# Performance work log

Hardware: AMD Instinct MI355X
Metric: run time of the kernel (lower is better)

The kernel has to match this reference:

```python
import jax, jax.numpy as jnp
import numpy as np

# static config (matches init_kwargs)
B, Q, D, H, L, P, V, T = 4, 32, 512, 8, 4, 4, 12000, 16
HD = D // H                      # attn_feat_dim = d_model / n_heads
TS = [2048, 1024, 512, 256]      # temporal_shapes (1-D feature pyramid)
LS = [0, 2048, 3072, 3584]       # level_start_index
S = sum(TS)


def setup_inputs() -> dict:
    key = jax.random.key(0)
    ks = jax.random.split(key, 20)
    f = jnp.float32
    def n(k, shape, s=0.02):
        return jax.random.normal(k, shape, dtype=f) * s
    return dict(
        seq_tokens=jax.random.randint(ks[0], (B * Q, T), 0, V),
        decoder_hidden_states=n(ks[1], (B, Q, D), 1.0),
        reference_points=jax.random.uniform(ks[2], (B, Q, 1), dtype=f),
        enc=n(ks[3], (B, S, D), 1.0),
        valid_ratios=jnp.ones((B, L), dtype=f),
        mask_flatten=jnp.zeros((B, S), dtype=bool),
        temporal_shapes=jnp.array(TS, dtype=jnp.int32),
        level_start_index=jnp.array(LS, dtype=jnp.int32),
        embed_W=jax.random.uniform(ks[4], (V, D), dtype=f, minval=-0.1, maxval=0.1),
        logit_W=jax.random.uniform(ks[5], (V, D), dtype=f, minval=-0.1, maxval=0.1),
        logit_b=jnp.zeros((V,), f),
        Wih=n(ks[6], (4 * D, 3 * D)),   # LSTM weight_ih (no bias), gate order i,f,g,o
        Whh=n(ks[7], (4 * D, D)),       # LSTM weight_hh
        value_W=n(ks[8], (D, D)), value_b=jnp.zeros((D,), f),
        off_W=n(ks[9], (H * L * P, 2 * D)), off_b=n(ks[10], (H * L * P,), 0.5),
        aw_W=n(ks[11], (H * L * P, 2 * D)), aw_b=jnp.zeros((H * L * P,), f),
        ctx_W=n(ks[12], (D, HD)), ctx_b=jnp.zeros((D,), f),
        hs_W=n(ks[13], (D, D)), hs_b=jnp.zeros((D,), f),
        alpha_W=n(ks[14], (1, D)), alpha_b=jnp.zeros((1,), f),
    )


def _forward(seq_tokens, decoder_hidden_states, reference_points, enc, valid_ratios,
             mask_flatten, temporal_shapes, level_start_index,
             embed_W, logit_W, logit_b, Wih, Whh, value_W, value_b,
             off_W, off_b, aw_W, aw_b, ctx_W, ctx_b, hs_W, hs_b, alpha_W, alpha_b):
    ts = [int(t) for t in np.asarray(temporal_shapes)]
    ls = [int(s) for s in np.asarray(level_start_index)]
    query = decoder_hidden_states            # (B, Q, D)
    BQ = B * Q
    # prepare_for_captioning: ref (B,Q,1) -> (B,Q,L,1) scaled by valid_ratios
    refp = reference_points[:, :, None, :] * valid_ratios[:, None, :, None]
    # value projection + padding mask
    value = jnp.where(mask_flatten[..., None], 0.0, enc @ value_W.T + value_b).reshape(B, S, H, HD)
    v_levels = [value[:, ls[l]:ls[l] + ts[l]].transpose(0, 2, 1, 3) for l in range(L)]  # (B,H,Tl,HD)
    ts_f = jnp.asarray(ts, dtype=query.dtype)

    def sample_level(v_l, loc, Tl):
        # 1-D linear interpolation, align_corners=False, zero padding (grid_sample style)
        # v_l: (B,H,Tl,HD); loc: (B,Q,H,P) normalized in [0,1]
        x = loc * Tl - 0.5
        x0 = jnp.floor(x)
        w = (x - x0)[..., None].transpose(0, 2, 1, 3, 4)   # (B,H,Q,P,1)
        i0 = x0.astype(jnp.int32)
        def gather(i):
            m = ((i >= 0) & (i < Tl))[..., None].astype(v_l.dtype).transpose(0, 2, 1, 3, 4)
            idx = jnp.clip(i, 0, Tl - 1).transpose(0, 2, 1, 3).reshape(B, H, Q * P)
            g = jnp.take_along_axis(v_l, idx[..., None], axis=2)  # (B,H,Q*P,HD)
            return g.reshape(B, H, Q, P, HD) * m
        return gather(i0) * (1.0 - w) + gather(i0 + 1) * w        # (B,H,Q,P,HD)

    def step(carry, tok):
        h, c = carry                                              # (BQ, D) each
        # TemporalMSDA query = cat(prev_h, query)
        hs_in = jnp.concatenate([h.reshape(B, Q, D), query], axis=2)       # (B,Q,2D)
        off = (hs_in @ off_W.T + off_b).reshape(B, Q, H, L, P)
        aw = jax.nn.softmax((hs_in @ aw_W.T + aw_b).reshape(B, Q, H, L * P), axis=-1)
        loc = refp[:, :, None, :, :] + off / ts_f[None, None, None, :, None]  # (B,Q,H,L,P)
        sampled = jnp.stack([sample_level(v_levels[l], loc[..., l, :], ts[l])
                             for l in range(L)], axis=3).reshape(B, H, Q, L * P, HD)
        weighted = sampled * aw.transpose(0, 2, 1, 3)[..., None]  # per-point MSDA-weighted values
        ctx = weighted.transpose(0, 2, 1, 3, 4).reshape(BQ, H, L * P, HD)
        # tanh additive attention over the L*P sampled points (per head)
        attn = ctx @ ctx_W.T + ctx_b                              # (BQ,H,LP,D)
        attn_h = (h @ hs_W.T + hs_b)[:, None, None, :]
        dot = (jnp.tanh(attn + attn_h) @ alpha_W.T + alpha_b)[..., 0]  # (BQ,H,LP)
        wgt = jax.nn.softmax(dot, axis=-1)
        attn_res = jnp.einsum('bhp,bhpd->bhd', wgt, ctx).reshape(BQ, D)
        # LSTM cell (bias=False), torch gate order i,f,g,o
        x = jnp.concatenate([embed_W[tok], attn_res, query.reshape(BQ, D)], axis=1)
        gates = x @ Wih.T + h @ Whh.T
        gi, gf, gg, go = jnp.split(gates, 4, axis=1)
        c2 = jax.nn.sigmoid(gf) * c + jax.nn.sigmoid(gi) * jnp.tanh(gg)
        h2 = jax.nn.sigmoid(go) * jnp.tanh(c2)
        return (h2, c2), jax.nn.log_softmax(h2 @ logit_W.T + logit_b, axis=-1)

    h0 = jnp.zeros((BQ, D), dtype=query.dtype)
    _, outs = jax.lax.scan(step, (h0, h0), seq_tokens[:, :-1].T)   # (T-1, BQ, V)
    return outs.transpose(1, 0, 2).reshape(B, Q, T - 1, V)


def reference(seq_tokens, decoder_hidden_states, reference_points, enc, valid_ratios,
              mask_flatten, temporal_shapes, level_start_index,
              embed_W, logit_W, logit_b, Wih, Whh, value_W, value_b,
              off_W, off_b, aw_W, aw_b, ctx_W, ctx_b, hs_W, hs_b, alpha_W, alpha_b):
    return _forward(seq_tokens, decoder_hidden_states, reference_points, enc, valid_ratios,
                    mask_flatten, temporal_shapes, level_start_index,
                    embed_W, logit_W, logit_b, Wih, Whh, value_W, value_b,
                    off_W, off_b, aw_W, aw_b, ctx_W, ctx_b, hs_W, hs_b, alpha_W, alpha_b)
```

## Files before the change

kernel.cpp:

```cpp
#include <hip/hip_runtime.h>

#define B_ 4
#define Q_ 32
#define D_ 512
#define H_ 8
#define L_ 4
#define P_ 4
#define V_ 12000
#define T_ 16
#define HD_ 64
#define S_ 3840
#define BQ_ 128
#define NSTEP 15
#define NSLAB 94

typedef __attribute__((ext_vector_type(8))) short short8;
typedef __attribute__((ext_vector_type(4))) float f32x4;

__device__ inline unsigned short f2bf(float x) {
  union { float f; unsigned u; } v; v.f = x;
  unsigned u = v.u;
  unsigned r = (u + 0x7fffu + ((u >> 16) & 1u)) >> 16;
  return (unsigned short)r;
}
__device__ inline float bf2f(unsigned short b) {
  union { unsigned u; float f; } v; v.u = ((unsigned)b) << 16; return v.f;
}
__device__ inline float fast_tanh(float x) {
  x = fminf(fmaxf(x, -15.f), 15.f);
  float e = __expf(2.f * x);
  return (e - 1.f) / (e + 1.f);
}
__device__ inline float sigmoidf_(float x) { return 1.f / (1.f + __expf(-x)); }

#define APAD 40
struct SmemGemm {
  unsigned short As0[128 * APAD], Bs0[128 * APAD];
  unsigned short As1[128 * APAD], Bs1[128 * APAD];
};
struct SmemGemmS {
  unsigned short As[128 * APAD], Bs[128 * APAD];
};
struct SmemSample {
  float ctx_s[16][HD_];
  unsigned short ctxbf[16][72];
  float aw_s[16];
  float wgt_s[16];
  float wred[4][16];
};

__device__ inline short8 cvt8(float4 v0, float4 v1) {
  short8 p;
  p[0] = (short)f2bf(v0.x); p[1] = (short)f2bf(v0.y);
  p[2] = (short)f2bf(v0.z); p[3] = (short)f2bf(v0.w);
  p[4] = (short)f2bf(v1.x); p[5] = (short)f2bf(v1.y);
  p[6] = (short)f2bf(v1.z); p[7] = (short)f2bf(v1.w);
  return p;
}

__device__ inline void mfma_step(const unsigned short* As, const unsigned short* Bs,
                                 f32x4 acc[4][4], int wm, int wn, int lane) {
  int r15 = lane & 15, koct = (lane >> 4) * 8;
  short8 a[4], b[4];
#pragma unroll
  for (int mf = 0; mf < 4; mf++)
    a[mf] = *(const short8*)(As + (wm * 64 + mf * 16 + r15) * APAD + koct);
#pragma unroll
  for (int nf = 0; nf < 4; nf++)
    b[nf] = *(const short8*)(Bs + (wn * 64 + nf * 16 + r15) * APAD + koct);
#pragma unroll
  for (int mf = 0; mf < 4; mf++)
#pragma unroll
    for (int nf = 0; nf < 4; nf++)
      acc[mf][nf] = __builtin_amdgcn_mfma_f32_16x16x32_bf16(a[mf], b[nf], acc[mf][nf], 0, 0, 0);
}

template <int NT, class FA, class FB>
__device__ inline void gemm_pipe(FA loadA, FB loadB, SmemGemm& sm,
                                 f32x4 acc[4][4], int wm, int wn, int lane, int tid) {
  int r = tid >> 2, ko = (tid & 3) * 8;
  short8 a0, a1, b0, b1;
  loadA(0, a0, a1); loadB(0, b0, b1);
#pragma unroll
  for (int t = 0; t < NT; t++) {
    unsigned short* As = (t & 1) ? sm.As1 : sm.As0;
    unsigned short* Bs = (t & 1) ? sm.Bs1 : sm.Bs0;
    *(short8*)(As + r * APAD + ko) = a0;
    *(short8*)(As + (r + 64) * APAD + ko) = a1;
    *(short8*)(Bs + r * APAD + ko) = b0;
    *(short8*)(Bs + (r + 64) * APAD + ko) = b1;
    short8 na0, na1, nb0, nb1;
    if (t + 1 < NT) { loadA(t + 1, na0, na1); loadB(t + 1, nb0, nb1); }
    __syncthreads();
    mfma_step(As, Bs, acc, wm, wn, lane);
    if (t + 1 < NT) { a0 = na0; a1 = na1; b0 = nb0; b1 = nb1; }
  }
}

template <int NT, class FA, class FB>
__device__ inline void gemm_simple(FA loadA, FB loadB, SmemGemmS& sm,
                                   f32x4 acc[4][4], int wm, int wn, int lane, int tid) {
  int r = tid >> 2, ko = (tid & 3) * 8;
#pragma unroll 2
  for (int t = 0; t < NT; t++) {
    short8 a0, a1, b0, b1;
    loadA(t, a0, a1); loadB(t, b0, b1);
    *(short8*)(sm.As + r * APAD + ko) = a0;
    *(short8*)(sm.As + (r + 64) * APAD + ko) = a1;
    *(short8*)(sm.Bs + r * APAD + ko) = b0;
    *(short8*)(sm.Bs + (r + 64) * APAD + ko) = b1;
    __syncthreads();
    mfma_step(sm.As, sm.Bs, acc, wm, wn, lane);
    __syncthreads();
  }
}

__device__ inline void mfma_epilogue(float* __restrict__ out, int ldo, int m0, int n0,
                                     int Nmax, const float* __restrict__ bias,
                                     const unsigned char* __restrict__ mask,
                                     const float* __restrict__ base,
                                     f32x4 acc[4][4], int wm, int wn, int lane) {
  int rb = (lane >> 4) * 4, cb = lane & 15;
#pragma unroll
  for (int nf = 0; nf < 4; nf++) {
    int col = n0 + wn * 64 + nf * 16 + cb;
    if (col >= Nmax) continue;
    float bv = bias ? bias[col] : 0.f;
#pragma unroll
    for (int mf = 0; mf < 4; mf++) {
#pragma unroll
      for (int j = 0; j < 4; j++) {
        int row = m0 + wm * 64 + mf * 16 + rb + j;
        float v = acc[mf][nf][j] + bv;
        if (base) v += base[(size_t)row * ldo + col];
        if (mask && mask[row]) v = 0.f;
        out[(size_t)row * ldo + col] = v;
      }
    }
  }
}

__device__ inline void mfma_epilogue_bf16(unsigned short* __restrict__ out, int ldo, int n0,
                                          f32x4 acc[4][4], int wm, int wn, int lane) {
  int rb = (lane >> 4) * 4, cb = lane & 15;
#pragma unroll
  for (int nf = 0; nf < 4; nf++) {
    int col = n0 + wn * 64 + nf * 16 + cb;
#pragma unroll
    for (int mf = 0; mf < 4; mf++) {
#pragma unroll
      for (int j = 0; j < 4; j++) {
        int row = wm * 64 + mf * 16 + rb + j;
        out[(size_t)row * ldo + col] = f2bf(acc[mf][nf][j]);
      }
    }
  }
}

#define ACC_INIT f32x4 acc[4][4]; { f32x4 z = {0.f,0.f,0.f,0.f}; \
  _Pragma("unroll") for (int i_=0;i_<4;i_++) _Pragma("unroll") for (int j_=0;j_<4;j_++) acc[i_][j_]=z; }


__global__ __launch_bounds__(256) void k_prep(const float* __restrict__ logitW,
    const float* __restrict__ Wih, const float* __restrict__ Whh,
    const float* __restrict__ offW, const float* __restrict__ awW,
    const float* __restrict__ hsW, const float* __restrict__ valueW,
    const float* __restrict__ query, const float* __restrict__ ctxW,
    const int* __restrict__ seq, const float* __restrict__ embedW,
    unsigned short* __restrict__ logitWbf, unsigned short* __restrict__ Wihbf,
    unsigned short* __restrict__ Whhbf, unsigned short* __restrict__ offWbf,
    unsigned short* __restrict__ awWbf, unsigned short* __restrict__ hsWbf,
    unsigned short* __restrict__ valueWbf, unsigned short* __restrict__ qbf,
    unsigned short* __restrict__ ctxWbf, unsigned short* __restrict__ hall,
    float* __restrict__ c0, unsigned short* __restrict__ xembbf) {
  int gi = blockIdx.x * 256 + threadIdx.x;
  const int e0 = 1536000, e1 = e0 + 786432, e2 = e1 + 262144, e3 = e2 + 32768,
            e4 = e3 + 32768, e5 = e4 + 65536, e6 = e5 + 65536, e7 = e6 + 16384;
  const int e8 = e7 + 16384, e9 = e8 + 8192, e10 = e9 + 245760;
  if (gi < e7) {
    const float* src; unsigned short* dst; int lo, dsti;
    if (gi < e0)      { src = logitW; dst = logitWbf; lo = gi; dsti = lo; }
    else if (gi < e1) {
      src = Wih; dst = Wihbf; lo = gi - e0;
      int row = lo / 384, c4 = lo - row * 384;
      int g = row >> 9, d = row & 511, n = d >> 5, rr = d & 31;
      dsti = (n * 128 + g * 32 + rr) * 384 + c4;
    }
    else if (gi < e2) {
      src = Whh; dst = Whhbf; lo = gi - e1;
      int row = lo >> 7, c4 = lo & 127;
      int g = row >> 9, d = row & 511, n = d >> 5, rr = d & 31;
      dsti = (n * 128 + g * 32 + rr) * 128 + c4;
    }
    else if (gi < e3) { src = offW;   dst = offWbf;   lo = gi - e2; dsti = lo; }
    else if (gi < e4) { src = awW;    dst = awWbf;    lo = gi - e3; dsti = lo; }
    else if (gi < e5) { src = hsW;    dst = hsWbf;    lo = gi - e4; dsti = lo; }
    else if (gi < e6) { src = valueW; dst = valueWbf; lo = gi - e5; dsti = lo; }
    else              { src = query;  dst = qbf;      lo = gi - e6; dsti = lo; }
    float4 v = ((const float4*)src)[lo];
    ushort4 o;
    o.x = f2bf(v.x); o.y = f2bf(v.y); o.z = f2bf(v.z); o.w = f2bf(v.w);
    ((ushort4*)dst)[dsti] = o;
  } else if (gi < e8) {
    int i = gi - e7;
    ushort4 z4; z4.x = 0; z4.y = 0; z4.z = 0; z4.w = 0;
    ((ushort4*)hall)[i] = z4;
    float4 z = {0.f, 0.f, 0.f, 0.f};
    ((float4*)c0)[i] = z;
  } else if (gi < e9) {
    int i = gi - e8;
    float4 v = ((const float4*)ctxW)[i];
    ushort4 o;
    o.x = f2bf(v.x); o.y = f2bf(v.y); o.z = f2bf(v.z); o.w = f2bf(v.w);
    ((ushort4*)ctxWbf)[i] = o;
  } else if (gi < e10) {
    int i = gi - e9;
    int row = i >> 7, d4 = i & 127;
    int t = row >> 7, bq = row & 127;
    int tok = seq[bq * T_ + t];
    float4 v = ((const float4*)embedW)[(size_t)tok * 128 + d4];
    ushort4 o;
    o.x = f2bf(v.x); o.y = f2bf(v.y); o.z = f2bf(v.z); o.w = f2bf(v.w);
    ((ushort4*)xembbf)[(size_t)row * 128 + d4] = o;
  }
}

__global__ __launch_bounds__(256) void k_value(const float* __restrict__ enc,
    const unsigned short* __restrict__ valueWbf, const float* __restrict__ valueb,
    const unsigned char* __restrict__ mask, float* __restrict__ value) {
  __shared__ SmemGemmS sm;
  int blk = blockIdx.x;
  int xcd = blk & 7, j = blk >> 3;
  int m0 = (xcd * 15 + (j >> 2)) * 128, n0 = (j & 3) * 128;
  int tid = threadIdx.x;
  int lane = tid & 63, w = tid >> 6, wm = w >> 1, wn = w & 1;
  int r = tid >> 2, ko = (tid & 3) * 8;
  ACC_INIT;
  gemm_simple<16>(
    [&](int t, short8& x, short8& y) {
      const float4* s0 = (const float4*)(enc + (size_t)(m0 + r) * 512 + t * 32 + ko);
      const float4* s1 = (const float4*)(enc + (size_t)(m0 + r + 64) * 512 + t * 32 + ko);
      x = cvt8(s0[0], s0[1]); y = cvt8(s1[0], s1[1]);
    },
    [&](int t, short8& x, short8& y) {
      x = *(const short8*)(valueWbf + (size_t)(n0 + r) * 512 + t * 32 + ko);
      y = *(const short8*)(valueWbf + (size_t)(n0 + r + 64) * 512 + t * 32 + ko);
    },
    sm, acc, wm, wn, lane, tid);
  mfma_epilogue(value, 512, m0, n0, 512, valueb, mask, nullptr, acc, wm, wn, lane);
}

__global__ __launch_bounds__(256) void k_qg(const unsigned short* __restrict__ qbf,
    const unsigned short* __restrict__ offWbf, const float* __restrict__ offb,
    const unsigned short* __restrict__ awWbf, const float* __restrict__ awb,
    float* __restrict__ off_base, float* __restrict__ aw_base,
    const unsigned short* __restrict__ xembbf,
    const unsigned short* __restrict__ Wihbf, unsigned short* __restrict__ gates_base) {
  __shared__ SmemGemmS sm;
  int blk = blockIdx.x;
  int tid = threadIdx.x;
  int lane = tid & 63, w = tid >> 6, wm = w >> 1, wn = w & 1;
  int r = tid >> 2, ko = (tid & 3) * 8;
  if (blk < 2) {
    const unsigned short* Bw = blk ? awWbf : offWbf;
    const float* bias = blk ? awb : offb;
    float* out = blk ? aw_base : off_base;
    ACC_INIT;
    gemm_simple<16>(
      [&](int t, short8& x, short8& y) {
        x = *(const short8*)(qbf + (size_t)r * 512 + t * 32 + ko);
        y = *(const short8*)(qbf + (size_t)(r + 64) * 512 + t * 32 + ko);
      },
      [&](int t, short8& x, short8& y) {
        x = *(const short8*)(Bw + (size_t)r * 1024 + 512 + t * 32 + ko);
        y = *(const short8*)(Bw + (size_t)(r + 64) * 1024 + 512 + t * 32 + ko);
      },
      sm, acc, wm, wn, lane, tid);
    mfma_epilogue(out, 128, 0, 0, 128, bias, nullptr, nullptr, acc, wm, wn, lane);
  } else {
    int g = blk - 2;
    int xcd = g & 7, j = g >> 3;
    int n0 = (xcd * 2 + (j >= 15)) * 128;
    int st = (j >= 15) ? (j - 15) : j;
    const unsigned short* xa = xembbf + (size_t)(st * 128) * 512;
    ACC_INIT;
    gemm_simple<32>(
      [&](int t, short8& x, short8& y) {
        const unsigned short* src = (t < 16) ? xa : qbf;
        int kk = (t < 16) ? t * 32 : (t - 16) * 32;
        x = *(const short8*)(src + (size_t)r * 512 + kk + ko);
        y = *(const short8*)(src + (size_t)(r + 64) * 512 + kk + ko);
      },
      [&](int t, short8& x, short8& y) {
        int kk = (t < 16) ? t * 32 : 1024 + (t - 16) * 32;
        x = *(const short8*)(Wihbf + (size_t)(n0 + r) * 1536 + kk + ko);
        y = *(const short8*)(Wihbf + (size_t)(n0 + r + 64) * 1536 + kk + ko);
      },
      sm, acc, wm, wn, lane, tid);
    mfma_epilogue_bf16(gates_base + (size_t)st * 128 * 2048, 2048, n0, acc, wm, wn, lane);
  }
}

__global__ __launch_bounds__(256) void k_sample(const float* __restrict__ value,
    const float* __restrict__ off_src, const float* __restrict__ aw_src,
    const float* __restrict__ hp_src, int hstride,
    const float* __restrict__ refp, const float* __restrict__ vrat,
    const unsigned short* __restrict__ ctxWbf, const float* __restrict__ ctxb,
    const float* __restrict__ alphaW, const float* __restrict__ alphab,
    unsigned short* __restrict__ attnbf) {
  __shared__ SmemSample sm;
  int blk = blockIdx.x;
  int bq = blk >> 3, h = blk & 7;
  int b = bq >> 5;
  int tid = threadIdx.x;
  int lane = tid & 63, wid = tid >> 6;

  if (tid < 16) {
    float v = aw_src[bq * 128 + h * 16 + tid];
    float m = v;
#pragma unroll
    for (int o = 8; o; o >>= 1) m = fmaxf(m, __shfl_xor(m, o, 16));
    float e = __expf(v - m);
    float s = e;
#pragma unroll
    for (int o = 8; o; o >>= 1) s += __shfl_xor(s, o, 16);
    sm.aw_s[tid] = e / s;
  }
  __syncthreads();

  {
    const int TSv[4] = {2048, 1024, 512, 256};
    const int LSv[4] = {0, 2048, 3072, 3584};
    float ref = refp[bq];
    int hd = tid & 63;
#pragma unroll
    for (int pp = 0; pp < 4; pp++) {
      int p = pp * 4 + (tid >> 6);
      int l = p >> 2;
      int Tl = TSv[l];
      float off = off_src[bq * 128 + h * 16 + p];
      float loc = ref * vrat[b * L_ + l] + off / (float)Tl;
      float x = loc * (float)Tl - 0.5f;
      float x0 = floorf(x);
      float wf = x - x0;
      int i0 = (int)x0;
      const float* vb = value + ((size_t)(b * S_ + LSv[l]) * D_) + h * HD_ + hd;
      float v0 = (i0 >= 0 && i0 < Tl) ? vb[(size_t)i0 * D_] : 0.f;
      float v1 = (i0 + 1 >= 0 && i0 + 1 < Tl) ? vb[(size_t)(i0 + 1) * D_] : 0.f;
      float cv = (v0 * (1.f - wf) + v1 * wf) * sm.aw_s[p];
      sm.ctx_s[p][hd] = cv;
      sm.ctxbf[p][hd] = f2bf(cv);
    }
  }
  __syncthreads();

  {
    int r15 = lane & 15, koct = (lane >> 4) * 8;
    int rb = (lane >> 4) * 4, cb = lane & 15;
    short8 a0 = *(const short8*)(&sm.ctxbf[r15][koct]);
    short8 a1 = *(const short8*)(&sm.ctxbf[r15][32 + koct]);
    float part0 = 0.f, part1 = 0.f, part2 = 0.f, part3 = 0.f;
#pragma unroll
    for (int nf = 0; nf < 8; nf++) {
      int d0 = wid * 128 + nf * 16;
      const unsigned short* bp = ctxWbf + (size_t)(d0 + r15) * 64;
      short8 b0 = *(const short8*)(bp + koct);
      short8 b1 = *(const short8*)(bp + 32 + koct);
      f32x4 acc = {0.f, 0.f, 0.f, 0.f};
      acc = __builtin_amdgcn_mfma_f32_16x16x32_bf16(a0, b0, acc, 0, 0, 0);
      acc = __builtin_amdgcn_mfma_f32_16x16x32_bf16(a1, b1, acc, 0, 0, 0);
      int d = d0 + cb;
      float add = ctxb[d] + hp_src[(size_t)hstride * bq + d];
      float al = alphaW[d];
      part0 += al * fast_tanh(acc[0] + add);
      part1 += al * fast_tanh(acc[1] + add);
      part2 += al * fast_tanh(acc[2] + add);
      part3 += al * fast_tanh(acc[3] + add);
    }
#pragma unroll
    for (int o = 8; o; o >>= 1) {
      part0 += __shfl_xor(part0, o, 16);
      part1 += __shfl_xor(part1, o, 16);
      part2 += __shfl_xor(part2, o, 16);
      part3 += __shfl_xor(part3, o, 16);
    }
    if (cb == 0) {
      sm.wred[wid][rb + 0] = part0;
      sm.wred[wid][rb + 1] = part1;
      sm.wred[wid][rb + 2] = part2;
      sm.wred[wid][rb + 3] = part3;
    }
  }
  __syncthreads();
  if (tid < 16) {
    float v = sm.wred[0][tid] + sm.wred[1][tid] + sm.wred[2][tid] + sm.wred[3][tid] + alphab[0];
    float m = v;
#pragma unroll
    for (int o = 8; o; o >>= 1) m = fmaxf(m, __shfl_xor(m, o, 16));
    float e = __expf(v - m);
    float s = e;
#pragma unroll
    for (int o = 8; o; o >>= 1) s += __shfl_xor(s, o, 16);
    sm.wgt_s[tid] = e / s;
  }
  __syncthreads();
  if (tid < 64) {
    float a = 0.f;
#pragma unroll
    for (int pi = 0; pi < 16; pi++) a += sm.wgt_s[pi] * sm.ctx_s[pi][tid];
    attnbf[bq * D_ + h * HD_ + tid] = f2bf(a);
  }
}

__global__ __launch_bounds__(256) void k_lstm_gemm(
    const unsigned short* __restrict__ attnbf, const unsigned short* __restrict__ hcur,
    const unsigned short* __restrict__ Wihbf, const unsigned short* __restrict__ Whhbf,
    float* __restrict__ gpart) {
  __shared__ SmemGemm sm;
  int tid = threadIdx.x;
  int lane = tid & 63, w = tid >> 6, wm = w >> 1, wn = w & 1;
  int r = tid >> 2, ko = (tid & 3) * 8;
  int n0 = blockIdx.x * 128;
  int kc = blockIdx.y;
  const unsigned short* Asrc = (kc < 2) ? (attnbf + kc * 256) : (hcur + (kc - 2) * 256);
  const unsigned short* Bsrc = (kc < 2) ? (Wihbf + (size_t)n0 * 1536 + 512 + kc * 256)
                                        : (Whhbf + (size_t)n0 * 512 + (kc - 2) * 256);
  int ldB = (kc < 2) ? 1536 : 512;
  ACC_INIT;
  gemm_pipe<8>(
    [&](int t, short8& x, short8& y) {
      x = *(const short8*)(Asrc + (size_t)r * 512 + t * 32 + ko);
      y = *(const short8*)(Asrc + (size_t)(r + 64) * 512 + t * 32 + ko);
    },
    [&](int t, short8& x, short8& y) {
      x = *(const short8*)(Bsrc + (size_t)r * ldB + t * 32 + ko);
      y = *(const short8*)(Bsrc + (size_t)(r + 64) * ldB + t * 32 + ko);
    },
    sm, acc, wm, wn, lane, tid);
  mfma_epilogue(gpart + (size_t)kc * 262144, 2048, 0, n0, 2048,
                nullptr, nullptr, nullptr, acc, wm, wn, lane);
}

__global__ __launch_bounds__(256) void k_cell(const float* __restrict__ gpart,
    const unsigned short* __restrict__ gbase_t,
    const float* __restrict__ c, float* __restrict__ cn, unsigned short* __restrict__ hout) {
  int idx = blockIdx.x * 256 + threadIdx.x;
  int bq = idx >> 9, d = idx & 511;
  int n = d >> 5, rr = d & 31;
  size_t rowoff = (size_t)bq * 2048 + n * 128 + rr;
  float g4[4];
#pragma unroll
  for (int gate = 0; gate < 4; gate++) {
    size_t off = rowoff + gate * 32;
    float s = bf2f(gbase_t[off]);
    s += gpart[off] + gpart[262144 + off] + gpart[2 * 262144 + off] + gpart[3 * 262144 + off];
    g4[gate] = s;
  }
  float cc = c[idx];
  float c2 = sigmoidf_(g4[1]) * cc + sigmoidf_(g4[0]) * fast_tanh(g4[2]);
  float h2 = sigmoidf_(g4[3]) * fast_tanh(c2);
  cn[idx] = c2;
  hout[idx] = f2bf(h2);
}

__global__ __launch_bounds__(256) void k_pre(const unsigned short* __restrict__ hbf,
    const unsigned short* __restrict__ offWbf, const unsigned short* __restrict__ awWbf,
    const unsigned short* __restrict__ hsWbf, const float* __restrict__ hsb,
    const float* __restrict__ off_base, const float* __restrict__ aw_base,
    float* __restrict__ offo, float* __restrict__ awo, float* __restrict__ hpo) {
  __shared__ SmemGemm sm;
  int blk = blockIdx.x;
  const unsigned short* Bw; const float* bias; const float* base;
  float* out; int ldkB, n0, ldo;
  if (blk == 0)      { Bw = offWbf; bias = nullptr; base = off_base; out = offo; ldkB = 1024; n0 = 0; ldo = 128; }
  else if (blk == 1) { Bw = awWbf;  bias = nullptr; base = aw_base;  out = awo;  ldkB = 1024; n0 = 0; ldo = 128; }
  else { Bw = hsWbf; bias = hsb; base = nullptr; out = hpo; ldkB = 512; n0 = (blk - 2) * 128; ldo = 512; }
  int tid = threadIdx.x;
  int lane = tid & 63, w = tid >> 6, wm = w >> 1, wn = w & 1;
  int r = tid >> 2, ko = (tid & 3) * 8;
  ACC_INIT;
  gemm_pipe<16>(
    [&](int t, short8& x, short8& y) {
      x = *(const short8*)(hbf + (size_t)r * 512 + t * 32 + ko);
      y = *(const short8*)(hbf + (size_t)(r + 64) * 512 + t * 32 + ko);
    },
    [&](int t, short8& x, short8& y) {
      x = *(const short8*)(Bw + (size_t)(n0 + r) * ldkB + t * 32 + ko);
      y = *(const short8*)(Bw + (size_t)(n0 + r + 64) * ldkB + t * 32 + ko);
    },
    sm, acc, wm, wn, lane, tid);
  mfma_epilogue(out, ldo, 0, n0, ldo, bias, nullptr, base, acc, wm, wn, lane);
}

__global__ __launch_bounds__(256) void k_logits_big(
    const unsigned short* __restrict__ logitWbf, const float* __restrict__ logitb,
    const unsigned short* __restrict__ hall, float* __restrict__ outp,
    float* __restrict__ m_sb, float* __restrict__ s_sb) {
  __shared__ SmemGemm sm;
  __shared__ float mred[128][2], sred[128][2];
  int blk = blockIdx.x;
  int swz = (blk & 7) * 177 + (blk >> 3);
  if (swz >= NSLAB * NSTEP) return;
  int slab = swz / NSTEP, t = swz % NSTEP;
  int n0 = slab * 128;
  int tid = threadIdx.x;
  int lane = tid & 63, w = tid >> 6, wm = w >> 1, wn = w & 1;
  int r = tid >> 2, ko = (tid & 3) * 8;
  const unsigned short* hn = hall + (size_t)(t + 1) * 65536;
  bool ok0 = (n0 + r) < V_, ok1 = (n0 + r + 64) < V_;
  ACC_INIT;
  gemm_pipe<16>(
    [&](int tt, short8& x, short8& y) {
      x = *(const short8*)(hn + (size_t)r * 512 + tt * 32 + ko);
      y = *(const short8*)(hn + (size_t)(r + 64) * 512 + tt * 32 + ko);
    },
    [&](int tt, short8& x, short8& y) {
      short8 z = {0, 0, 0, 0, 0, 0, 0, 0};
      x = ok0 ? *(const short8*)(logitWbf + (size_t)(n0 + r) * 512 + tt * 32 + ko) : z;
      y = ok1 ? *(const short8*)(logitWbf + (size_t)(n0 + r + 64) * 512 + tt * 32 + ko) : z;
    },
    sm, acc, wm, wn, lane, tid);
  int rb = (lane >> 4) * 4, cb = lane & 15;
#pragma unroll
  for (int mf = 0; mf < 4; mf++) {
#pragma unroll
    for (int j = 0; j < 4; j++) {
      int row = wm * 64 + mf * 16 + rb + j;
      float vv[4];
      float mx = -3.4e38f;
#pragma unroll
      for (int nf = 0; nf < 4; nf++) {
        int col = n0 + wn * 64 + nf * 16 + cb;
        bool ok = col < V_;
        float v = ok ? (acc[mf][nf][j] + logitb[col]) : -3.4e38f;
        if (ok) outp[((size_t)row * NSTEP + t) * V_ + col] = v;
        vv[nf] = v;
        mx = fmaxf(mx, v);
      }
#pragma unroll
      for (int o = 8; o; o >>= 1) mx = fmaxf(mx, __shfl_xor(mx, o, 16));
      float sme = 0.f;
#pragma unroll
      for (int nf = 0; nf < 4; nf++) sme += (vv[nf] > -3.0e38f) ? __expf(vv[nf] - mx) : 0.f;
#pragma unroll
      for (int o = 8; o; o >>= 1) sme += __shfl_xor(sme, o, 16);
      if (cb == 0) { mred[row][wn] = mx; sred[row][wn] = sme; }
    }
  }
  __syncthreads();
  if (tid < 128) {
    float m0 = mred[tid][0], m1 = mred[tid][1];
    float M = fmaxf(m0, m1);
    float Ssum = sred[tid][0] * __expf(m0 - M) + sred[tid][1] * __expf(m1 - M);
    m_sb[((size_t)t * 128 + tid) * 96 + slab] = M;
    s_sb[((size_t)t * 128 + tid) * 96 + slab] = Ssum;
  }
}

__global__ __launch_bounds__(256) void k_out_all(const float* __restrict__ m_sb,
    const float* __restrict__ s_sb, float* __restrict__ outp) {
  __shared__ float ms[NSLAB], ss[NSLAB];
  __shared__ float lse_s;
  int blk = blockIdx.x;
  int t = blk >> 7, row = blk & 127;
  int tid = threadIdx.x;
  size_t pbase = ((size_t)t * 128 + row) * 96;
  if (tid < NSLAB) { ms[tid] = m_sb[pbase + tid]; ss[tid] = s_sb[pbase + tid]; }
  __syncthreads();
  if (tid < 64) {
    float m = -3.4e38f, s = 0.f;
    for (int i = tid; i < NSLAB; i += 64) {
      float mi = ms[i], si = ss[i];
      float M = fmaxf(m, mi);
      s = s * __expf(m - M) + si * __expf(mi - M);
      m = M;
    }
#pragma unroll
    for (int o = 32; o; o >>= 1) {
      float mo = __shfl_xor(m, o, 64), so = __shfl_xor(s, o, 64);
      float M = fmaxf(m, mo);
      s = s * __expf(m - M) + so * __expf(mo - M);
      m = M;
    }
    if (tid == 0) lse_s = m + __logf(s);
  }
  __syncthreads();
  float lse = lse_s;
  float4* op = (float4*)(outp + ((size_t)row * NSTEP + t) * V_);
  for (int i = tid; i < V_ / 4; i += 256) {
    float4 v = op[i];
    v.x -= lse; v.y -= lse; v.z -= lse; v.w -= lse;
    op[i] = v;
  }
}

extern "C" void kernel_launch(void* const* d_in, const int* in_sizes, int n_in,
                              void* d_out, int out_size, void* d_ws, size_t ws_size,
                              hipStream_t stream) {
  const int* seq             = (const int*)d_in[0];
  const float* query         = (const float*)d_in[1];
  const float* refp          = (const float*)d_in[2];
  const float* enc           = (const float*)d_in[3];
  const float* vrat          = (const float*)d_in[4];
  const unsigned char* mask  = (const unsigned char*)d_in[5];
  const float* embedW        = (const float*)d_in[8];
  const float* logitW        = (const float*)d_in[9];
  const float* logitb        = (const float*)d_in[10];
  const float* Wih           = (const float*)d_in[11];
  const float* Whh           = (const float*)d_in[12];
  const float* valueW        = (const float*)d_in[13];
  const float* valueb        = (const float*)d_in[14];
  const float* offW          = (const float*)d_in[15];
  const float* offb          = (const float*)d_in[16];
  const float* awW           = (const float*)d_in[17];
  const float* awb           = (const float*)d_in[18];
  const float* ctxW          = (const float*)d_in[19];
  const float* ctxb          = (const float*)d_in[20];
  const float* hsW           = (const float*)d_in[21];
  const float* hsb           = (const float*)d_in[22];
  const float* alphaW        = (const float*)d_in[23];
  const float* alphab        = (const float*)d_in[24];

  char* wp = (char*)d_ws;
  auto alloc_f = [&](size_t n) { float* p = (float*)wp; wp += ((n * 4 + 255) / 256) * 256; return p; };
  auto alloc_u = [&](size_t n) { unsigned short* p = (unsigned short*)wp; wp += ((n * 2 + 255) / 256) * 256; return p; };

  float* value   = alloc_f((size_t)B_ * S_ * D_);
  float* gpart   = alloc_f((size_t)4 * BQ_ * 2048);
  float* hproj   = alloc_f((size_t)BQ_ * D_);
  float* offo    = alloc_f((size_t)BQ_ * 128);
  float* awo     = alloc_f((size_t)BQ_ * 128);
  float* off_base= alloc_f((size_t)BQ_ * 128);
  float* aw_base = alloc_f((size_t)BQ_ * 128);
  float* c0      = alloc_f((size_t)BQ_ * D_);
  float* c1      = alloc_f((size_t)BQ_ * D_);
  float* m_sb    = alloc_f((size_t)NSTEP * BQ_ * 96);
  float* s_sb    = alloc_f((size_t)NSTEP * BQ_ * 96);
  unsigned short* hall    = alloc_u((size_t)(NSTEP + 1) * BQ_ * D_);
  unsigned short* attnbf  = alloc_u((size_t)BQ_ * D_);
  unsigned short* qbf     = alloc_u((size_t)BQ_ * D_);
  unsigned short* ctxWbf  = alloc_u((size_t)512 * 64);
  unsigned short* xembbf  = alloc_u((size_t)NSTEP * BQ_ * D_);
  unsigned short* gates_base = alloc_u((size_t)NSTEP * BQ_ * 2048);
  unsigned short* logitWbf = alloc_u((size_t)V_ * D_);
  unsigned short* Wihbf    = alloc_u((size_t)2048 * 1536);
  unsigned short* Whhbf    = alloc_u((size_t)2048 * 512);
  unsigned short* offWbf   = alloc_u((size_t)128 * 1024);
  unsigned short* awWbf    = alloc_u((size_t)128 * 1024);
  unsigned short* hsWbf    = alloc_u((size_t)512 * 512);
  unsigned short* valueWbf = alloc_u((size_t)512 * 512);

  k_prep<<<11984, 256, 0, stream>>>(logitW, Wih, Whh, offW, awW, hsW, valueW, query, ctxW,
                                    seq, embedW,
                                    logitWbf, Wihbf, Whhbf, offWbf, awWbf, hsWbf,
                                    valueWbf, qbf, ctxWbf, hall, c0, xembbf);
  k_value<<<480, 256, 0, stream>>>(enc, valueWbf, valueb, mask, value);
  k_qg<<<242, 256, 0, stream>>>(qbf, offWbf, offb, awWbf, awb, off_base, aw_base,
                                xembbf, Wihbf, gates_base);

  float* cb[2] = {c0, c1};
  float* outp = (float*)d_out;

  for (int t = 0; t < NSTEP; t++) {
    const unsigned short* hcur = hall + (size_t)t * BQ_ * D_;
    unsigned short* hnxt = hall + (size_t)(t + 1) * BQ_ * D_;
    if (t == 0)
      k_sample<<<1024, 256, 0, stream>>>(value, off_base, aw_base, hsb, 0, refp, vrat,
                                         ctxWbf, ctxb, alphaW, alphab, attnbf);
    else
      k_sample<<<1024, 256, 0, stream>>>(value, offo, awo, hproj, 512, refp, vrat,
                                         ctxWbf, ctxb, alphaW, alphab, attnbf);
    k_lstm_gemm<<<dim3(16, 4), 256, 0, stream>>>(attnbf, hcur, Wihbf, Whhbf, gpart);
    k_cell<<<256, 256, 0, stream>>>(gpart, gates_base + (size_t)t * BQ_ * 2048,
                                    cb[t & 1], cb[(t + 1) & 1], hnxt);
    if (t + 1 < NSTEP)
      k_pre<<<6, 256, 0, stream>>>(hnxt, offWbf, awWbf, hsWbf, hsb,
                                   off_base, aw_base, offo, awo, hproj);
  }

  k_logits_big<<<1416, 256, 0, stream>>>(logitWbf, logitb, hall, outp, m_sb, s_sb);
  k_out_all<<<NSTEP * BQ_, 256, 0, stream>>>(m_sb, s_sb, outp);
}
```

Before: 760.2 us.

## Fuse LSTM gate GEMM with cell update and merge one-time setup kernels

```diff
diff --git a/kernel.cpp b/kernel.cpp
--- a/kernel.cpp
+++ b/kernel.cpp
@@ -225,32 +225,10 @@
   }
 }
 
-__global__ __launch_bounds__(256) void k_value(const float* __restrict__ enc,
+__global__ __launch_bounds__(256) void k_onetime(const float* __restrict__ enc,
     const unsigned short* __restrict__ valueWbf, const float* __restrict__ valueb,
-    const unsigned char* __restrict__ mask, float* __restrict__ value) {
-  __shared__ SmemGemmS sm;
-  int blk = blockIdx.x;
-  int xcd = blk & 7, j = blk >> 3;
-  int m0 = (xcd * 15 + (j >> 2)) * 128, n0 = (j & 3) * 128;
-  int tid = threadIdx.x;
-  int lane = tid & 63, w = tid >> 6, wm = w >> 1, wn = w & 1;
-  int r = tid >> 2, ko = (tid & 3) * 8;
-  ACC_INIT;
-  gemm_simple<16>(
-    [&](int t, short8& x, short8& y) {
-      const float4* s0 = (const float4*)(enc + (size_t)(m0 + r) * 512 + t * 32 + ko);
-      const float4* s1 = (const float4*)(enc + (size_t)(m0 + r + 64) * 512 + t * 32 + ko);
-      x = cvt8(s0[0], s0[1]); y = cvt8(s1[0], s1[1]);
-    },
-    [&](int t, short8& x, short8& y) {
-      x = *(const short8*)(valueWbf + (size_t)(n0 + r) * 512 + t * 32 + ko);
-      y = *(const short8*)(valueWbf + (size_t)(n0 + r + 64) * 512 + t * 32 + ko);
-    },
-    sm, acc, wm, wn, lane, tid);
-  mfma_epilogue(value, 512, m0, n0, 512, valueb, mask, nullptr, acc, wm, wn, lane);
-}
-
-__global__ __launch_bounds__(256) void k_qg(const unsigned short* __restrict__ qbf,
+    const unsigned char* __restrict__ mask, float* __restrict__ value,
+    const unsigned short* __restrict__ qbf,
     const unsigned short* __restrict__ offWbf, const float* __restrict__ offb,
     const unsigned short* __restrict__ awWbf, const float* __restrict__ awb,
     float* __restrict__ off_base, float* __restrict__ aw_base,
@@ -261,10 +239,26 @@
   int tid = threadIdx.x;
   int lane = tid & 63, w = tid >> 6, wm = w >> 1, wn = w & 1;
   int r = tid >> 2, ko = (tid & 3) * 8;
-  if (blk < 2) {
-    const unsigned short* Bw = blk ? awWbf : offWbf;
-    const float* bias = blk ? awb : offb;
-    float* out = blk ? aw_base : off_base;
+  if (blk < 480) {
+    int xcd = blk & 7, j = blk >> 3;
+    int m0 = (xcd * 15 + (j >> 2)) * 128, n0 = (j & 3) * 128;
+    ACC_INIT;
+    gemm_simple<16>(
+      [&](int t, short8& x, short8& y) {
+        const float4* s0 = (const float4*)(enc + (size_t)(m0 + r) * 512 + t * 32 + ko);
+        const float4* s1 = (const float4*)(enc + (size_t)(m0 + r + 64) * 512 + t * 32 + ko);
+        x = cvt8(s0[0], s0[1]); y = cvt8(s1[0], s1[1]);
+      },
+      [&](int t, short8& x, short8& y) {
+        x = *(const short8*)(valueWbf + (size_t)(n0 + r) * 512 + t * 32 + ko);
+        y = *(const short8*)(valueWbf + (size_t)(n0 + r + 64) * 512 + t * 32 + ko);
+      },
+      sm, acc, wm, wn, lane, tid);
+    mfma_epilogue(value, 512, m0, n0, 512, valueb, mask, nullptr, acc, wm, wn, lane);
+  } else if (blk < 482) {
+    const unsigned short* Bw = (blk == 481) ? awWbf : offWbf;
+    const float* bias = (blk == 481) ? awb : offb;
+    float* out = (blk == 481) ? aw_base : off_base;
     ACC_INIT;
     gemm_simple<16>(
       [&](int t, short8& x, short8& y) {
@@ -278,7 +272,7 @@
       sm, acc, wm, wn, lane, tid);
     mfma_epilogue(out, 128, 0, 0, 128, bias, nullptr, nullptr, acc, wm, wn, lane);
   } else {
-    int g = blk - 2;
+    int g = blk - 482;
     int xcd = g & 7, j = g >> 3;
     int n0 = (xcd * 2 + (j >= 15)) * 128;
     int st = (j >= 15) ? (j - 15) : j;
@@ -412,55 +406,99 @@
   }
 }
 
-__global__ __launch_bounds__(256) void k_lstm_gemm(
+__global__ __launch_bounds__(256) void k_lstm_cell(
     const unsigned short* __restrict__ attnbf, const unsigned short* __restrict__ hcur,
     const unsigned short* __restrict__ Wihbf, const unsigned short* __restrict__ Whhbf,
-    float* __restrict__ gpart) {
-  __shared__ SmemGemm sm;
+    const unsigned short* __restrict__ gbase_t,
+    const float* __restrict__ c, float* __restrict__ cn,
+    unsigned short* __restrict__ hout) {
+  __shared__ unsigned short As[2][32 * APAD];
+  __shared__ unsigned short Bs[2][128 * APAD];
+  __shared__ float gs[32][132];
   int tid = threadIdx.x;
   int lane = tid & 63, w = tid >> 6, wm = w >> 1, wn = w & 1;
-  int r = tid >> 2, ko = (tid & 3) * 8;
-  int n0 = blockIdx.x * 128;
-  int kc = blockIdx.y;
-  const unsigned short* Asrc = (kc < 2) ? (attnbf + kc * 256) : (hcur + (kc - 2) * 256);
-  const unsigned short* Bsrc = (kc < 2) ? (Wihbf + (size_t)n0 * 1536 + 512 + kc * 256)
-                                        : (Whhbf + (size_t)n0 * 512 + (kc - 2) * 256);
-  int ldB = (kc < 2) ? 1536 : 512;
-  ACC_INIT;
-  gemm_pipe<8>(
-    [&](int t, short8& x, short8& y) {
-      x = *(const short8*)(Asrc + (size_t)r * 512 + t * 32 + ko);
-      y = *(const short8*)(Asrc + (size_t)(r + 64) * 512 + t * 32 + ko);
-    },
-    [&](int t, short8& x, short8& y) {
-      x = *(const short8*)(Bsrc + (size_t)r * ldB + t * 32 + ko);
-      y = *(const short8*)(Bsrc + (size_t)(r + 64) * ldB + t * 32 + ko);
-    },
-    sm, acc, wm, wn, lane, tid);
-  mfma_epilogue(gpart + (size_t)kc * 262144, 2048, 0, n0, 2048,
-                nullptr, nullptr, nullptr, acc, wm, wn, lane);
-}
-
-__global__ __launch_bounds__(256) void k_cell(const float* __restrict__ gpart,
-    const unsigned short* __restrict__ gbase_t,
-    const float* __restrict__ c, float* __restrict__ cn, unsigned short* __restrict__ hout) {
-  int idx = blockIdx.x * 256 + threadIdx.x;
-  int bq = idx >> 9, d = idx & 511;
-  int n = d >> 5, rr = d & 31;
-  size_t rowoff = (size_t)bq * 2048 + n * 128 + rr;
-  float g4[4];
-#pragma unroll
-  for (int gate = 0; gate < 4; gate++) {
-    size_t off = rowoff + gate * 32;
-    float s = bf2f(gbase_t[off]);
-    s += gpart[off] + gpart[262144 + off] + gpart[2 * 262144 + off] + gpart[3 * 262144 + off];
-    g4[gate] = s;
-  }
-  float cc = c[idx];
-  float c2 = sigmoidf_(g4[1]) * cc + sigmoidf_(g4[0]) * fast_tanh(g4[2]);
-  float h2 = sigmoidf_(g4[3]) * fast_tanh(c2);
-  cn[idx] = c2;
-  hout[idx] = f2bf(h2);
+  int blk = blockIdx.x;
+  int m0 = (blk >> 4) * 32, nb = blk & 15, n0 = nb * 128;
+  int r15 = lane & 15, koct = (lane >> 4) * 8;
+
+  auto loadA = [&](int t, short8& x) {
+    if (tid < 128) {
+      int r = tid >> 2, ko = (tid & 3) * 8;
+      int kg = t * 32;
+      const unsigned short* src = (kg < 512) ? (attnbf + kg) : (hcur + kg - 512);
+      x = *(const short8*)(src + (size_t)(m0 + r) * 512 + ko);
+    }
+  };
+  auto loadB = [&](int t, short8& x, short8& y) {
+    int kg = t * 32;
+    const unsigned short* src; size_t ldB;
+    if (kg < 512) { src = Wihbf + (size_t)n0 * 1536 + 512 + kg; ldB = 1536; }
+    else          { src = Whhbf + (size_t)n0 * 512 + (kg - 512); ldB = 512; }
+    int i0 = tid, i1 = tid + 256;
+    x = *(const short8*)(src + (size_t)(i0 >> 2) * ldB + (i0 & 3) * 8);
+    y = *(const short8*)(src + (size_t)(i1 >> 2) * ldB + (i1 & 3) * 8);
+  };
+
+  f32x4 acc[4];
+  { f32x4 z = {0.f, 0.f, 0.f, 0.f};
+#pragma unroll
+    for (int i = 0; i < 4; i++) acc[i] = z; }
+
+  short8 a_reg, b_reg0, b_reg1;
+  loadA(0, a_reg); loadB(0, b_reg0, b_reg1);
+#pragma unroll 2
+  for (int t = 0; t < 32; t++) {
+    unsigned short* Ab = As[t & 1];
+    unsigned short* Bb = Bs[t & 1];
+    if (tid < 128) {
+      int r = tid >> 2, ko = (tid & 3) * 8;
+      *(short8*)(Ab + r * APAD + ko) = a_reg;
+    }
+    {
+      int i0 = tid, i1 = tid + 256;
+      *(short8*)(Bb + (i0 >> 2) * APAD + (i0 & 3) * 8) = b_reg0;
+      *(short8*)(Bb + (i1 >> 2) * APAD + (i1 & 3) * 8) = b_reg1;
+    }
+    short8 na, nb0, nb1;
+    if (t + 1 < 32) { loadA(t + 1, na); loadB(t + 1, nb0, nb1); }
+    __syncthreads();
+    short8 af = *(const short8*)(Ab + (wm * 16 + r15) * APAD + koct);
+#pragma unroll
+    for (int nf = 0; nf < 4; nf++) {
+      short8 bfrag = *(const short8*)(Bb + (wn * 64 + nf * 16 + r15) * APAD + koct);
+      acc[nf] = __builtin_amdgcn_mfma_f32_16x16x32_bf16(af, bfrag, acc[nf], 0, 0, 0);
+    }
+    __syncthreads();
+    if (t + 1 < 32) { a_reg = na; b_reg0 = nb0; b_reg1 = nb1; }
+  }
+
+  {
+    int rb = (lane >> 4) * 4, cb = lane & 15;
+#pragma unroll
+    for (int nf = 0; nf < 4; nf++) {
+      int col = wn * 64 + nf * 16 + cb;
+#pragma unroll
+      for (int j = 0; j < 4; j++)
+        gs[wm * 16 + rb + j][col] = acc[nf][j];
+    }
+  }
+  __syncthreads();
+#pragma unroll
+  for (int i = 0; i < 4; i++) {
+    int idx = i * 256 + tid;
+    int lr = idx >> 5, rr = idx & 31;
+    size_t gb = (size_t)(m0 + lr) * 2048 + n0 + rr;
+    float gi = gs[lr][rr]      + bf2f(gbase_t[gb]);
+    float gf = gs[lr][32 + rr] + bf2f(gbase_t[gb + 32]);
+    float gg = gs[lr][64 + rr] + bf2f(gbase_t[gb + 64]);
+    float go = gs[lr][96 + rr] + bf2f(gbase_t[gb + 96]);
+    int gidx = (m0 + lr) * 512 + nb * 32 + rr;
+    float cc = c[gidx];
+    float c2 = sigmoidf_(gf) * cc + sigmoidf_(gi) * fast_tanh(gg);
+    float h2 = sigmoidf_(go) * fast_tanh(c2);
+    cn[gidx] = c2;
+    hout[gidx] = f2bf(h2);
+  }
 }
 
 __global__ __launch_bounds__(256) void k_pre(const unsigned short* __restrict__ hbf,
@@ -496,7 +534,7 @@
     const unsigned short* __restrict__ logitWbf, const float* __restrict__ logitb,
     const unsigned short* __restrict__ hall, float* __restrict__ outp,
     float* __restrict__ m_sb, float* __restrict__ s_sb) {
-  __shared__ SmemGemm sm;
+  __shared__ SmemGemmS sm;
   __shared__ float mred[128][2], sred[128][2];
   int blk = blockIdx.x;
   int swz = (blk & 7) * 177 + (blk >> 3);
@@ -509,7 +547,7 @@
   const unsigned short* hn = hall + (size_t)(t + 1) * 65536;
   bool ok0 = (n0 + r) < V_, ok1 = (n0 + r + 64) < V_;
   ACC_INIT;
-  gemm_pipe<16>(
+  gemm_simple<16>(
     [&](int tt, short8& x, short8& y) {
       x = *(const short8*)(hn + (size_t)r * 512 + tt * 32 + ko);
       y = *(const short8*)(hn + (size_t)(r + 64) * 512 + tt * 32 + ko);
@@ -626,7 +664,6 @@
   auto alloc_u = [&](size_t n) { unsigned short* p = (unsigned short*)wp; wp += ((n * 2 + 255) / 256) * 256; return p; };
 
   float* value   = alloc_f((size_t)B_ * S_ * D_);
-  float* gpart   = alloc_f((size_t)4 * BQ_ * 2048);
   float* hproj   = alloc_f((size_t)BQ_ * D_);
   float* offo    = alloc_f((size_t)BQ_ * 128);
   float* awo     = alloc_f((size_t)BQ_ * 128);
@@ -654,9 +691,9 @@
                                     seq, embedW,
                                     logitWbf, Wihbf, Whhbf, offWbf, awWbf, hsWbf,
                                     valueWbf, qbf, ctxWbf, hall, c0, xembbf);
-  k_value<<<480, 256, 0, stream>>>(enc, valueWbf, valueb, mask, value);
-  k_qg<<<242, 256, 0, stream>>>(qbf, offWbf, offb, awWbf, awb, off_base, aw_base,
-                                xembbf, Wihbf, gates_base);
+  k_onetime<<<722, 256, 0, stream>>>(enc, valueWbf, valueb, mask, value,
+                                     qbf, offWbf, offb, awWbf, awb, off_base, aw_base,
+                                     xembbf, Wihbf, gates_base);
 
   float* cb[2] = {c0, c1};
   float* outp = (float*)d_out;
@@ -670,9 +707,9 @@
     else
       k_sample<<<1024, 256, 0, stream>>>(value, offo, awo, hproj, 512, refp, vrat,
                                          ctxWbf, ctxb, alphaW, alphab, attnbf);
-    k_lstm_gemm<<<dim3(16, 4), 256, 0, stream>>>(attnbf, hcur, Wihbf, Whhbf, gpart);
-    k_cell<<<256, 256, 0, stream>>>(gpart, gates_base + (size_t)t * BQ_ * 2048,
-                                    cb[t & 1], cb[(t + 1) & 1], hnxt);
+    k_lstm_cell<<<64, 256, 0, stream>>>(attnbf, hcur, Wihbf, Whhbf,
+                                        gates_base + (size_t)t * BQ_ * 2048,
+                                        cb[t & 1], cb[(t + 1) & 1], hnxt);
     if (t + 1 < NSTEP)
       k_pre<<<6, 256, 0, stream>>>(hnxt, offWbf, awWbf, hsWbf, hsb,
                                    off_base, aw_base, offo, awo, hproj);
```

Result: slower. 834.4 us (+9.8%).
